# Performance work log

Measured on AMD Instinct MI355X. Metric: run time of the kernel, lower is better.

## Reference

```python
import jax, jax.numpy as jnp
import numpy as np

jax.config.update("jax_enable_x64", True)

N = 3
NX = (N ** 2) ** 3          # 729 decision vars (flattened 9x9x9 one-hot board)
M2 = 128                    # dense inequality rows (G2)
QPEN = 0.1                  # Qpenalty -> Q = QPEN * I
NITER = 10                  # fixed interior-point iterations
SIGMA = 0.1                 # centering parameter
B = 16                      # batch of puzzles


def setup_inputs() -> dict:
    key = jax.random.key(0)
    k1, k2 = jax.random.split(key)
    puzzles = jax.random.uniform(k1, (B, 9, 9, 9), dtype=jnp.float32)
    G2 = jax.random.uniform(k2, (M2, NX), minval=-1.0, maxval=1.0, dtype=jnp.float32)
    z2 = jnp.zeros((NX,), jnp.float32)
    s2 = jnp.ones((M2,), jnp.float32)
    return {"puzzles": puzzles, "G2": G2, "z2": z2, "s2": s2}


def _qp_solve(p, G2, h):
    """Solve min 0.5 z'Qz + p'z  s.t. [-I; G2] z <= h for a batch of p.

    Primal-dual interior-point method, fixed NITER steps, exploiting the
    block structure G = [-I; G2]:  G' D G = diag(d1) + G2' D2 G2.
    p: (B, NX) float64. Returns z: (B, NX).
    """
    Bn, nx = p.shape
    G = jnp.concatenate([-jnp.eye(nx, dtype=p.dtype), G2], axis=0)  # (m, nx)
    m = G.shape[0]
    eye = jnp.eye(nx, dtype=p.dtype)

    z0 = jnp.zeros((Bn, nx), p.dtype)
    s0 = jnp.ones((Bn, m), p.dtype)
    lam0 = jnp.ones((Bn, m), p.dtype)

    def maxstep(x, dx):
        # largest alpha<=1 keeping x + alpha*dx > 0 (fraction-to-boundary 0.99)
        ratio = jnp.where(dx < 0, -x / jnp.where(dx < 0, dx, -1.0), jnp.inf)
        return jnp.minimum(1.0, 0.99 * jnp.min(ratio, axis=1))

    def step(carry, _):
        z, s, lam = carry
        Gz = z @ G.T                                   # (B, m)
        rd = QPEN * z + p + lam @ G                    # dual residual (B, nx)
        rp = Gz + s - h                                # primal residual (B, m)
        mu = jnp.mean(s * lam, axis=1, keepdims=True)  # (B, 1)
        d = lam / s                                    # (B, m)
        v = SIGMA * mu / s - lam + d * rp              # (B, m)
        rhs = -(rd + v @ G)                            # (B, nx)
        # K = Q + G' D G = diag(QPEN + d1) + G2' D2 G2  (block-sparse structure)
        K = jnp.einsum('mi,bm,mj->bij', G2, d[:, nx:], G2)
        K = K + eye[None] * (QPEN + d[:, :nx])[:, :, None]
        dz = jnp.linalg.solve(K, rhs[..., None])[..., 0]
        Gdz = dz @ G.T
        ds = -rp - Gdz
        dlam = v + d * Gdz
        alpha = jnp.minimum(maxstep(s, ds), maxstep(lam, dlam))[:, None]
        return (z + alpha * dz, s + alpha * ds, lam + alpha * dlam), None

    (z, _, _), _ = jax.lax.scan(step, (z0, s0, lam0), None, length=NITER)
    return z


def reference(puzzles, G2, z2, s2):
    Bn = puzzles.shape[0]
    G2d = G2.astype(jnp.float64)
    z2d = z2.astype(jnp.float64)
    s2d = s2.astype(jnp.float64)
    p = -puzzles.reshape(Bn, -1).astype(jnp.float64)     # (B, NX)
    h2 = G2d @ z2d + s2d                                 # (M2,)
    h = jnp.concatenate([jnp.zeros(NX, jnp.float64), h2])
    z = _qp_solve(p, G2d, h)
    return z.astype(jnp.float32).reshape(puzzles.shape)
```

## Files before the change

kernel.cpp:

```cpp
#include <hip/hip_runtime.h>
#include <math.h>

#define NXQ 729
#define M2Q 128
#define MQ  857
#define BQ  16
#define QPEN_ 0.1
#define SIGMA_ 0.1

typedef double d4 __attribute__((ext_vector_type(4)));

constexpr int OFF_P    = 0;
constexpr int OFF_H2   = OFF_P + BQ*NXQ;
constexpr int OFF_Q2   = OFF_H2 + M2Q;
constexpr int OFF_TP   = OFF_Q2 + BQ*M2Q;
constexpr int ST_Z    = 0;
constexpr int ST_S    = 729;
constexpr int ST_LAM  = 1586;
constexpr int ST_RP   = 2443;
constexpr int ST_V    = 3300;
constexpr int ST_AINV = 4157;
constexpr int ST_Y    = 4886;
constexpr int ST_GZ   = 5615;
constexpr int STB     = 5743;
constexpr int OFF_ST  = OFF_TP + 12*BQ*M2Q;
constexpr int SGB_B   = 10240;
constexpr int OFF_SG  = OFF_ST + 2*BQ*STB;

constexpr int L_SL   = 0;
constexpr int L_US   = 16512;
constexpr int L_INVD = 16640;
constexpr int L_RED2 = 16768;
constexpr int SH_FUSED = (16768 + 544) * 8;
constexpr int D_DZ   = 0;
constexpr int D_RED  = 736;
constexpr int D_SC   = 744;
constexpr int D_Q2   = 752;
constexpr int D_YL   = 880;
constexpr int D_SN   = 944;
constexpr int D_LN   = 1801;
constexpr int D_PART = 2658;
constexpr int D_AINV = 12672;
constexpr int AR_W   = 1056;
constexpr int SH_PS  = 8448 * 8;

__device__ __constant__ int TRI_R[10] = {0,1,1,2,2,2,3,3,3,3};
__device__ __constant__ int TRI_C[10] = {0,0,1,0,1,2,0,1,2,3};
__device__ __constant__ int TRL_R[28] = {0,1,1,2,2,2,3,3,3,3,4,4,4,4,4,5,5,5,5,5,5,6,6,6,6,6,6,6};
__device__ __constant__ int TRL_C[28] = {0,0,1,0,1,2,0,1,2,3,0,1,2,3,4,0,1,2,3,4,5,0,1,2,3,4,5,6};

__device__ __forceinline__ double wred_sum(double v) {
#pragma unroll
  for (int off = 32; off > 0; off >>= 1) v += __shfl_down(v, off, 64);
  return v;
}
__device__ __forceinline__ double wred_min(double v) {
#pragma unroll
  for (int off = 32; off > 0; off >>= 1) v = fmin(v, __shfl_down(v, off, 64));
  return v;
}
__device__ __forceinline__ double rsqrt64(double x) {
  double r = (double)rsqrtf((float)x);
  r = r * (1.5 - 0.5 * x * r * r);
  r = r * (1.5 - 0.5 * x * r * r);
  return r;
}

__device__ __forceinline__ void mfma_cdmap(int* rowm, int* colm) {
  const int lane = threadIdx.x & 63;
  const int rc = lane & 15, kq = lane >> 4;
  const double avr = (kq == 0) ? (double)rc : 0.0;
  const double bv1 = (kq == 0) ? 1.0 : 0.0;
  const double av1 = (kq == 0) ? 1.0 : 0.0;
  const double bvc = (kq == 0) ? (double)rc : 0.0;
  d4 zero = {0.0, 0.0, 0.0, 0.0};
  d4 dr = __builtin_amdgcn_mfma_f64_16x16x4f64(avr, bv1, zero, 0, 0, 0);
  d4 dc = __builtin_amdgcn_mfma_f64_16x16x4f64(av1, bvc, zero, 0, 0, 0);
#pragma unroll
  for (int e = 0; e < 4; ++e) { rowm[e] = (int)dr[e]; colm[e] = (int)dc[e]; }
}

__global__ __launch_bounds__(512)
void init_kernel(const float* __restrict__ puzzles, const float* __restrict__ G2,
                 const float* __restrict__ z2in, const float* __restrict__ s2in,
                 double* __restrict__ ws) {
  const int blk = blockIdx.x;
  const int tid = threadIdx.x, wave = tid >> 6, lane = tid & 63;
  __shared__ double sm[32];
  if (blk < BQ) {
    const int bb = blk;
    double* st = ws + OFF_ST + bb * STB;
    for (int i = tid; i < NXQ; i += 512) {
      ws[OFF_P + bb * NXQ + i] = -(double)puzzles[bb * NXQ + i];
      st[ST_Z + i] = 0.0;
      st[ST_AINV + i] = 1.0 / (QPEN_ + 1.0);
      st[ST_RP + i] = 1.0;
      st[ST_V + i] = SIGMA_;
    }
    for (int i = tid; i < MQ; i += 512) { st[ST_S + i] = 1.0; st[ST_LAM + i] = 1.0; }
    if (tid < M2Q) st[ST_GZ + tid] = 0.0;
  } else {
    const int r = blk - 16;
    double acc = 0.0;
    for (int kx = tid; kx < NXQ; kx += 512)
      acc += (double)G2[r * NXQ + kx] * (double)z2in[kx];
    acc = wred_sum(acc);
    if (lane == 0) sm[wave] = acc;
    __syncthreads();
    if (tid == 0) {
      double t = 0.0;
#pragma unroll
      for (int w = 0; w < 8; ++w) t += sm[w];
      const double h2r = t + (double)s2in[r];
      ws[OFF_H2 + r] = h2r;
      sm[16] = h2r;
    }
    __syncthreads();
    if (tid < BQ) {
      double* st = ws + OFF_ST + tid * STB;
      const double rp2 = 1.0 - sm[16];
      st[ST_RP + NXQ + r] = rp2;
      st[ST_V  + NXQ + r] = rp2 - 0.9;
      ws[OFF_Q2 + tid * M2Q + r] = rp2 + 0.1;
    }
  }
}

__device__ __forceinline__ void sbuild_tile8(const float* __restrict__ G2,
                                             const double* __restrict__ ainv,
                                             double* __restrict__ arena,
                                             double* __restrict__ Sgb, const int tile,
                                             const int* rowm, const int* colm) {
  const int tid = threadIdx.x, wave = tid >> 6, lane = tid & 63;
  const int R0 = TRI_R[tile] * 32, C0 = TRI_C[tile] * 32;
  double* As = arena + wave * AR_W;
  double* Bs = As + 528;
  const int kw0 = wave * 92;
  const int kwend = min(kw0 + 92, NXQ);
  const int kk16 = lane & 15, rsub = lane >> 4;
  const int rc = lane & 15, kq = lane >> 4;
  d4 c00 = {0.0, 0.0, 0.0, 0.0}, c01 = c00, c10 = c00, c11 = c00;
  float pa[8], pb[8];
  {
    const int k = kw0 + kk16;
    const int kc = (k < kwend) ? k : (kwend - 1);
#pragma unroll
    for (int it = 0; it < 8; ++it) {
      const int rr = it * 4 + rsub;
      pa[it] = G2[(R0 + rr) * NXQ + kc];
      pb[it] = G2[(C0 + rr) * NXQ + kc];
    }
  }
  for (int ch = 0; ch < 6; ++ch) {
    {
      const int k = kw0 + ch * 16 + kk16;
      const bool ok = (k < kwend);
      const double aik = ok ? ainv[k] : 0.0;
#pragma unroll
      for (int it = 0; it < 8; ++it) {
        const int rr = it * 4 + rsub;
        As[kk16 * 33 + rr] = ok ? (double)pa[it] * aik : 0.0;
        Bs[kk16 * 33 + rr] = ok ? (double)pb[it] : 0.0;
      }
    }
    if (ch < 5) {
      const int k = kw0 + (ch + 1) * 16 + kk16;
      const int kc = (k < kwend) ? k : (kwend - 1);
#pragma unroll
      for (int it = 0; it < 8; ++it) {
        const int rr = it * 4 + rsub;
        pa[it] = G2[(R0 + rr) * NXQ + kc];
        pb[it] = G2[(C0 + rr) * NXQ + kc];
      }
    }
#pragma unroll
    for (int s = 0; s < 4; ++s) {
      const int ko = (s * 4 + kq) * 33;
      const double a0 = As[ko + rc], a1 = As[ko + 16 + rc];
      const double b0 = Bs[ko + rc], b1 = Bs[ko + 16 + rc];
      c00 = __builtin_amdgcn_mfma_f64_16x16x4f64(a0, b0, c00, 0, 0, 0);
      c01 = __builtin_amdgcn_mfma_f64_16x16x4f64(a0, b1, c01, 0, 0, 0);
      c10 = __builtin_amdgcn_mfma_f64_16x16x4f64(a1, b0, c10, 0, 0, 0);
      c11 = __builtin_amdgcn_mfma_f64_16x16x4f64(a1, b1, c11, 0, 0, 0);
    }
  }
  double* Wp = arena + wave * AR_W;
#pragma unroll
  for (int e = 0; e < 4; ++e) {
    Wp[rowm[e] * 33 + colm[e]]             = c00[e];
    Wp[rowm[e] * 33 + 16 + colm[e]]        = c01[e];
    Wp[(16 + rowm[e]) * 33 + colm[e]]      = c10[e];
    Wp[(16 + rowm[e]) * 33 + 16 + colm[e]] = c11[e];
  }
  __syncthreads();
  for (int idx = tid; idx < 1024; idx += 512) {
    const int r = idx >> 5, c = idx & 31;
    const int o = r * 33 + c;
    double v = arena[o];
#pragma unroll
    for (int w = 1; w < 8; ++w) v += arena[w * AR_W + o];
    Sgb[tile * 1024 + idx] = v;
  }
}

__global__ __launch_bounds__(512)
void ps_kernel(const float* __restrict__ G2, double* __restrict__ ws) {
  const int b = blockIdx.x, y = blockIdx.y;
  const int tid = threadIdx.x, lane = tid & 63;
  extern __shared__ double sm[];
  double* st = ws + OFF_ST + b * STB;
  if (y < 12) {
    double* uvec = sm;
    double* part = sm + 128;
    double* yl   = sm + 640;
    const int c0 = y * 64;
    if (tid < M2Q) uvec[tid] = ws[OFF_Q2 + b * M2Q + tid];
    __syncthreads();
    const int kk = tid & 63, rq = tid >> 6;
    const int k = c0 + kk;
    const int kg = (k < NXQ) ? k : (NXQ - 1);
    {
      const float* gp = G2 + (rq * 16) * NXQ + kg;
      double acc = 0.0;
#pragma unroll
      for (int j = 0; j < 16; ++j) acc = fma((double)gp[j * NXQ], uvec[rq * 16 + j], acc);
      part[rq * 64 + kk] = acc;
    }
    __syncthreads();
    if (tid < 64) {
      const int k2 = c0 + tid;
      double yv = 0.0;
      if (k2 < NXQ) {
        double w = 0.0;
#pragma unroll
        for (int q = 0; q < 8; ++q) w += part[q * 64 + tid];
        const double rhsk = -(QPEN_ * st[ST_Z + k2] + ws[OFF_P + b * NXQ + k2]
                              - st[ST_LAM + k2] - st[ST_V + k2] + w);
        yv = st[ST_AINV + k2] * rhsk;
        st[ST_Y + k2] = yv;
      }
      yl[tid] = yv;
    }
    __syncthreads();
    {
      const double yv = yl[lane];
      double pp[16];
#pragma unroll
      for (int jr = 0; jr < 16; ++jr)
        pp[jr] = (double)G2[((tid >> 6) * 16 + jr) * NXQ + kg] * yv;
#pragma unroll
      for (int st2 = 0; st2 < 4; ++st2) {
        const int m = 32 >> st2, half = 8 >> st2;
        const bool hi = (lane & m) != 0;
#pragma unroll
        for (int r = 0; r < 8; ++r) {
          if (r < half) {
            const double send = hi ? pp[r] : pp[r + half];
            const double recv = __shfl_xor(send, m, 64);
            pp[r] = (hi ? pp[r + half] : pp[r]) + recv;
          }
        }
      }
      double tot = pp[0];
      tot += __shfl_xor(tot, 2, 64);
      tot += __shfl_xor(tot, 1, 64);
      if ((lane & 3) == 0)
        ws[OFF_TP + (y * BQ + b) * M2Q + (tid >> 6) * 16 + ((lane >> 2) & 15)] = tot;
    }
    __syncthreads();
  }
  if (y >= 6) {
    int rowm[4], colm[4];
    mfma_cdmap(rowm, colm);
    sbuild_tile8(G2, st + ST_AINV, sm, ws + OFF_SG + b * SGB_B, y - 6,
                 rowm, colm);
  }
}

__global__ __launch_bounds__(512, 1)
void dps_kernel(const float* __restrict__ G2, double* __restrict__ ws,
                float* __restrict__ out, const int ph, const int last) {
  const int b = blockIdx.x, chunk = blockIdx.y;
  const int tid = threadIdx.x, wave = tid >> 6, lane = tid & 63;
  extern __shared__ double sm[];
  double (*Sl)[129] = (double(*)[129])(sm + L_SL);
  double* us   = sm + L_US;
  double* invd = sm + L_INVD;
  double* red2 = sm + L_RED2;
  const double* R = ws + OFF_ST + ph * BQ * STB + b * STB;
  double*       W = ws + OFF_ST + (1 - ph) * BQ * STB + b * STB;
  double* Sgb  = ws + OFF_SG + b * SGB_B;
  const int c0 = chunk * 64;

#pragma unroll
  for (int t = 0; t < 10; ++t) {
    const int R0 = TRI_R[t] * 32, C0 = TRI_C[t] * 32;
    const bool dg = (R0 == C0);
    for (int e = tid; e < 1024; e += 512) {
      const int r = e >> 5, c = e & 31;
      double v = Sgb[t * 1024 + e];
      if (dg && r == c) {
        const int i = C0 + c;
        v += R[ST_S + NXQ + i] / R[ST_LAM + NXQ + i];
      }
      Sl[R0 + r][C0 + c] = v;
    }
  }
  if (tid < M2Q) {
    double t = 0.0;
#pragma unroll
    for (int c = 0; c < 12; ++c) t += ws[OFF_TP + (c * BQ + b) * M2Q + tid];
    us[tid] = t;
  }
  __syncthreads();

  int rowm[4], colm[4];
  mfma_cdmap(rowm, colm);
  const int rc16 = lane & 15, kq4 = lane >> 4;

  auto panel16 = [&](const int K0) {
    const int r = lane;
    double a[16];
#pragma unroll
    for (int c = 0; c < 16; ++c) a[c] = Sl[K0 + r][K0 + c];
#pragma unroll
    for (int c = 0; c < 16; ++c) {
      const double dcc = __shfl(a[c], c, 64);
      const double rs = rsqrt64(dcc);
      a[c] *= rs;
      if (lane == c) invd[K0 + c] = rs;
#pragma unroll
      for (int k2 = c + 1; k2 < 16; ++k2) {
        const double lkc = __shfl(a[c], k2, 64);
        a[k2] = fma(-a[c], lkc, a[k2]);
      }
    }
#pragma unroll
    for (int c = 0; c < 16; ++c) Sl[K0 + r][K0 + c] = a[c];
  };

  auto tile_upd = [&](const int K0, const int i0, const int j0) {
    d4 tacc;
#pragma unroll
    for (int e = 0; e < 4; ++e) tacc[e] = Sl[i0 + rowm[e]][j0 + colm[e]];
#pragma unroll
    for (int m = 0; m < 4; ++m) {
      const double av = -Sl[i0 + rc16][K0 + 4 * m + kq4];
      const double bv =  Sl[j0 + rc16][K0 + 4 * m + kq4];
      tacc = __builtin_amdgcn_mfma_f64_16x16x4f64(av, bv, tacc, 0, 0, 0);
    }
#pragma unroll
    for (int e = 0; e < 4; ++e) Sl[i0 + rowm[e]][j0 + colm[e]] = tacc[e];
  };

  if (wave == 0 && lane < 16) panel16(0);
  __syncthreads();

  for (int kb = 0; kb < 8; ++kb) {
    const int K0 = kb * 16, J0 = K0 + 16, T = 128 - J0;
    if (tid <= T) {
      const bool isU = (tid == T);
      double l[16];
      if (isU) {
#pragma unroll
        for (int c = 0; c < 16; ++c) l[c] = us[K0 + c];
      } else {
#pragma unroll
        for (int c = 0; c < 16; ++c) l[c] = Sl[J0 + tid][K0 + c];
      }
#pragma unroll
      for (int c = 0; c < 16; ++c) {
        const double lc = l[c] * invd[K0 + c];
        l[c] = lc;
#pragma unroll
        for (int k2 = c + 1; k2 < 16; ++k2)
          l[k2] = fma(-lc, Sl[K0 + k2][K0 + c], l[k2]);
      }
      if (isU) {
#pragma unroll
        for (int c = 0; c < 16; ++c) us[K0 + c] = l[c];
      } else {
#pragma unroll
        for (int c = 0; c < 16; ++c) Sl[J0 + tid][K0 + c] = l[c];
      }
    }
    __syncthreads();

    if (kb < 7) {
      if (tid < T) {
        double acc = 0.0;
#pragma unroll
        for (int c = 0; c < 16; ++c) acc = fma(Sl[J0 + tid][K0 + c], us[K0 + c], acc);
        us[J0 + tid] -= acc;
      }
      if (wave == 7) tile_upd(K0, J0, J0);
      __syncthreads();
      const int Tb = 7 - kb;
      const int nt = (Tb * (Tb + 1)) >> 1;
      if (wave == 0) {
        if (lane < 16) panel16(J0);
      } else {
        for (int idx = wave; idx < nt; idx += 7)
          tile_upd(K0, J0 + TRL_R[idx] * 16, J0 + TRL_C[idx] * 16);
      }
      __syncthreads();
    }
  }

  for (int kb = 7; kb >= 0; --kb) {
    const int K0 = kb * 16;
    if (kb < 7) {
      const int c = tid & 15, ch = tid >> 4;
      double part = 0.0;
      for (int k = K0 + 16 + ch; k < 128; k += 32) part = fma(Sl[k][K0 + c], us[k], part);
      red2[ch * 17 + c] = part;
    }
    __syncthreads();
    if (wave == 0 && lane < 16) {
      const int j = lane;
      double x = us[K0 + j];
      if (kb < 7) {
        double acc = 0.0;
#pragma unroll
        for (int q = 0; q < 32; ++q) acc += red2[q * 17 + j];
        x -= acc;
      }
      double colv[16];
#pragma unroll
      for (int c = 0; c < 16; ++c) colv[c] = Sl[K0 + c][K0 + j];
      const double iv = invd[K0 + j];
#pragma unroll
      for (int cc = 0; cc < 16; ++cc) {
        const int c = 15 - cc;
        const double xiv = x * iv;
        const double uc = __shfl(xiv, c, 64);
        if (j == c) x = xiv;
        else if (j < c) x = fma(-colv[c], uc, x);
      }
      us[K0 + j] = x;
    }
    __syncthreads();
  }
  if (tid < M2Q) invd[tid] = (R[ST_S + NXQ + tid] / R[ST_LAM + NXQ + tid]) * us[tid];
  __syncthreads();
  double* g2b = invd;

  double* dzl   = sm + D_DZ;
  double* red   = sm + D_RED;
  double* sc    = sm + D_SC;
  double* ainvn = sm + D_AINV;
  double* q2l   = sm + D_Q2;
  double* yl    = sm + D_YL;
  double* snew  = sm + D_SN;
  double* lnew  = sm + D_LN;
  double* part  = sm + D_PART;

  double lmin = 1e300;
  for (int k = tid; k < NXQ; k += 512) {
    double accv = 0.0;
    const float* gp = G2 + k;
#pragma unroll 16
    for (int r = 0; r < M2Q; ++r) accv = fma((double)gp[r * NXQ], us[r], accv);
    const double dzv = R[ST_Y + k] - R[ST_AINV + k] * accv;
    dzl[k] = dzv;
    const double si = R[ST_S + k], li = R[ST_LAM + k], di = li / si;
    const double dsi = dzv - R[ST_RP + k];
    const double dlami = R[ST_V + k] - di * dzv;
    snew[k] = dsi; lnew[k] = dlami;
    if (dsi < 0.0)   lmin = fmin(lmin, -si / dsi);
    if (dlami < 0.0) lmin = fmin(lmin, -li / dlami);
  }
  if (tid >= 384) {
    const int m = tid - 384;
    const int i = NXQ + m;
    const double si = R[ST_S + i], li = R[ST_LAM + i], di = li / si;
    const double g = g2b[m];
    const double dsi = -R[ST_RP + i] - g;
    const double dlami = R[ST_V + i] + di * g;
    snew[i] = dsi; lnew[i] = dlami;
    if (dsi < 0.0)   lmin = fmin(lmin, -si / dsi);
    if (dlami < 0.0) lmin = fmin(lmin, -li / dlami);
  }
  lmin = wred_min(lmin);
  if (lane == 0) red[wave] = lmin;
  __syncthreads();
  if (tid == 0) {
    double m = red[0];
#pragma unroll
    for (int w = 1; w < 8; ++w) m = fmin(m, red[w]);
    sc[0] = fmin(1.0, 0.99 * m);
  }
  __syncthreads();
  const double alpha = sc[0];

  if (last) {
    const int k2 = c0 + (tid & 63);
    if (tid < 64 && k2 < NXQ)
      out[b * NXQ + k2] = (float)(R[ST_Z + k2] + alpha * dzl[k2]);
    return;
  }

  double musum = 0.0;
  for (int i = tid; i < MQ; i += 512) {
    const double si = R[ST_S + i], li = R[ST_LAM + i];
    const double sn = si + alpha * snew[i], ln = li + alpha * lnew[i];
    snew[i] = sn; lnew[i] = ln;
    musum += sn * ln;
  }
  musum = wred_sum(musum);
  if (lane == 0) red[wave] = musum;
  __syncthreads();
  if (tid == 0) {
    double t = 0.0;
#pragma unroll
    for (int w = 0; w < 8; ++w) t += red[w];
    sc[1] = SIGMA_ * (t / (double)MQ);
  }
  __syncthreads();
  const double smu = sc[1];

  for (int i = tid; i < MQ; i += 512) {
    const double sn = snew[i], ln = lnew[i], di = ln / sn;
    if (i < NXQ) {
      const double zn = R[ST_Z + i] + alpha * dzl[i];
      const double rpn = sn - zn;
      const double vn = smu / sn - ln + di * rpn;
      const double an = 1.0 / (QPEN_ + di);
      ainvn[i] = an;
      if ((i >> 6) == chunk) {
        W[ST_Z + i] = zn; W[ST_S + i] = sn; W[ST_LAM + i] = ln;
        W[ST_RP + i] = rpn; W[ST_V + i] = vn; W[ST_AINV + i] = an;
      }
    } else {
      const int m = i - NXQ;
      const double gzn = R[ST_GZ + m] + alpha * g2b[m];
      const double rpn = gzn + sn - ws[OFF_H2 + m];
      const double vn = smu / sn - ln + di * rpn;
      q2l[m] = ln + vn;
      if (chunk == 0) {
        W[ST_S + i] = sn; W[ST_LAM + i] = ln;
        W[ST_RP + i] = rpn; W[ST_V + i] = vn; W[ST_GZ + m] = gzn;
      }
    }
  }
  __syncthreads();

  if (chunk < 12) {
    const int kk = tid & 63, rq = tid >> 6;
    const int k = c0 + kk;
    const int kg = (k < NXQ) ? k : (NXQ - 1);
    {
      const float* gp = G2 + (rq * 16) * NXQ + kg;
      double acc = 0.0;
#pragma unroll
      for (int j = 0; j < 16; ++j) acc = fma((double)gp[j * NXQ], q2l[rq * 16 + j], acc);
      part[rq * 64 + kk] = acc;
    }
    __syncthreads();
    if (tid < 64) {
      const int k2 = c0 + tid;
      double y = 0.0;
      if (k2 < NXQ) {
        double w = 0.0;
#pragma unroll
        for (int q = 0; q < 8; ++q) w += part[q * 64 + tid];
        const double sn = snew[k2], ln = lnew[k2], di = ln / sn;
        const double zn = R[ST_Z + k2] + alpha * dzl[k2];
        const double rpn = sn - zn;
        const double vn = smu / sn - ln + di * rpn;
        const double rhsk = -(QPEN_ * zn + ws[OFF_P + b * NXQ + k2] - ln - vn + w);
        y = ainvn[k2] * rhsk;
        W[ST_Y + k2] = y;
      }
      yl[tid] = y;
    }
    __syncthreads();
    {
      const double yv = yl[lane];
      double pp[16];
#pragma unroll
      for (int jr = 0; jr < 16; ++jr)
        pp[jr] = (double)G2[((tid >> 6) * 16 + jr) * NXQ + kg] * yv;
#pragma unroll
      for (int st2 = 0; st2 < 4; ++st2) {
        const int m = 32 >> st2, half = 8 >> st2;
        const bool hi = (lane & m) != 0;
#pragma unroll
        for (int r = 0; r < 8; ++r) {
          if (r < half) {
            const double send = hi ? pp[r] : pp[r + half];
            const double recv = __shfl_xor(send, m, 64);
            pp[r] = (hi ? pp[r + half] : pp[r]) + recv;
          }
        }
      }
      double tot = pp[0];
      tot += __shfl_xor(tot, 2, 64);
      tot += __shfl_xor(tot, 1, 64);
      if ((lane & 3) == 0)
        ws[OFF_TP + (chunk * BQ + b) * M2Q + (tid >> 6) * 16 + ((lane >> 2) & 15)] = tot;
    }
    __syncthreads();
  }

  if (chunk >= 6)
    sbuild_tile8(G2, ainvn, sm, Sgb, chunk - 6, rowm, colm);
}

extern "C" void kernel_launch(void* const* d_in, const int* in_sizes, int n_in,
                              void* d_out, int out_size, void* d_ws, size_t ws_size,
                              hipStream_t stream) {
  const float* puzzles = (const float*)d_in[0];
  const float* G2      = (const float*)d_in[1];
  const float* z2      = (const float*)d_in[2];
  const float* s2      = (const float*)d_in[3];
  float* out = (float*)d_out;
  double* ws = (double*)d_ws;

  (void)hipFuncSetAttribute(reinterpret_cast<const void*>(&dps_kernel),
                            hipFuncAttributeMaxDynamicSharedMemorySize, SH_FUSED);
  (void)hipFuncSetAttribute(reinterpret_cast<const void*>(&ps_kernel),
                            hipFuncAttributeMaxDynamicSharedMemorySize, SH_PS);

  init_kernel<<<dim3(16 + M2Q), dim3(512), 0, stream>>>(puzzles, G2, z2, s2, ws);
  ps_kernel<<<dim3(BQ, 16), dim3(512), SH_PS, stream>>>(G2, ws);
  for (int it = 0; it < 10; ++it) {
    const int ph = it & 1;
    dps_kernel<<<dim3(BQ, 16), dim3(512), SH_FUSED, stream>>>(G2, ws, out, ph, (it == 9) ? 1 : 0);
  }
}
```

Before: 832.7 us.

## Widen dps_kernel to 1024 threads and spread tile updates over sixteen waves

Doubles the dps_kernel block from 512 to 1024 threads. The S-matrix load, the step-length and mu reductions, and the per-element state update become single-pass (one element per thread), and the blocked Cholesky tile updates are spread across 15 worker waves instead of 7. Several phases are guarded to the first 512 threads, and sbuild_tile8 is guarded to eight waves. Shared-memory offsets are shifted so the reduction scratch can hold 16 wave partials. The aim is more parallelism per block during the serial factorisation and elementwise phases, at the cost of register pressure from the 1024-thread bound and extra idle threads in the guarded phases.

New measurement: 1.153 ms. 1.38x slower.

```diff
diff --git a/kernel.cpp b/kernel.cpp
--- a/kernel.cpp
+++ b/kernel.cpp
@@ -34,12 +34,12 @@
 constexpr int SH_FUSED = (16768 + 544) * 8;
 constexpr int D_DZ   = 0;
 constexpr int D_RED  = 736;
-constexpr int D_SC   = 744;
-constexpr int D_Q2   = 752;
-constexpr int D_YL   = 880;
-constexpr int D_SN   = 944;
-constexpr int D_LN   = 1801;
-constexpr int D_PART = 2658;
+constexpr int D_SC   = 752;
+constexpr int D_Q2   = 760;
+constexpr int D_YL   = 888;
+constexpr int D_SN   = 952;
+constexpr int D_LN   = 1812;
+constexpr int D_PART = 2672;
 constexpr int D_AINV = 12672;
 constexpr int AR_W   = 1056;
 constexpr int SH_PS  = 8448 * 8;
@@ -133,38 +133,17 @@
                                              const int* rowm, const int* colm) {
   const int tid = threadIdx.x, wave = tid >> 6, lane = tid & 63;
   const int R0 = TRI_R[tile] * 32, C0 = TRI_C[tile] * 32;
-  double* As = arena + wave * AR_W;
-  double* Bs = As + 528;
-  const int kw0 = wave * 92;
-  const int kwend = min(kw0 + 92, NXQ);
-  const int kk16 = lane & 15, rsub = lane >> 4;
-  const int rc = lane & 15, kq = lane >> 4;
-  d4 c00 = {0.0, 0.0, 0.0, 0.0}, c01 = c00, c10 = c00, c11 = c00;
-  float pa[8], pb[8];
-  {
-    const int k = kw0 + kk16;
-    const int kc = (k < kwend) ? k : (kwend - 1);
-#pragma unroll
-    for (int it = 0; it < 8; ++it) {
-      const int rr = it * 4 + rsub;
-      pa[it] = G2[(R0 + rr) * NXQ + kc];
-      pb[it] = G2[(C0 + rr) * NXQ + kc];
-    }
-  }
-  for (int ch = 0; ch < 6; ++ch) {
+  if (wave < 8) {
+    double* As = arena + wave * AR_W;
+    double* Bs = As + 528;
+    const int kw0 = wave * 92;
+    const int kwend = min(kw0 + 92, NXQ);
+    const int kk16 = lane & 15, rsub = lane >> 4;
+    const int rc = lane & 15, kq = lane >> 4;
+    d4 c00 = {0.0, 0.0, 0.0, 0.0}, c01 = c00, c10 = c00, c11 = c00;
+    float pa[8], pb[8];
     {
-      const int k = kw0 + ch * 16 + kk16;
-      const bool ok = (k < kwend);
-      const double aik = ok ? ainv[k] : 0.0;
-#pragma unroll
-      for (int it = 0; it < 8; ++it) {
-        const int rr = it * 4 + rsub;
-        As[kk16 * 33 + rr] = ok ? (double)pa[it] * aik : 0.0;
-        Bs[kk16 * 33 + rr] = ok ? (double)pb[it] : 0.0;
-      }
-    }
-    if (ch < 5) {
-      const int k = kw0 + (ch + 1) * 16 + kk16;
+      const int k = kw0 + kk16;
       const int kc = (k < kwend) ? k : (kwend - 1);
 #pragma unroll
       for (int it = 0; it < 8; ++it) {
@@ -173,27 +152,50 @@
         pb[it] = G2[(C0 + rr) * NXQ + kc];
       }
     }
-#pragma unroll
-    for (int s = 0; s < 4; ++s) {
-      const int ko = (s * 4 + kq) * 33;
-      const double a0 = As[ko + rc], a1 = As[ko + 16 + rc];
-      const double b0 = Bs[ko + rc], b1 = Bs[ko + 16 + rc];
-      c00 = __builtin_amdgcn_mfma_f64_16x16x4f64(a0, b0, c00, 0, 0, 0);
-      c01 = __builtin_amdgcn_mfma_f64_16x16x4f64(a0, b1, c01, 0, 0, 0);
-      c10 = __builtin_amdgcn_mfma_f64_16x16x4f64(a1, b0, c10, 0, 0, 0);
-      c11 = __builtin_amdgcn_mfma_f64_16x16x4f64(a1, b1, c11, 0, 0, 0);
-    }
-  }
-  double* Wp = arena + wave * AR_W;
-#pragma unroll
-  for (int e = 0; e < 4; ++e) {
-    Wp[rowm[e] * 33 + colm[e]]             = c00[e];
-    Wp[rowm[e] * 33 + 16 + colm[e]]        = c01[e];
-    Wp[(16 + rowm[e]) * 33 + colm[e]]      = c10[e];
-    Wp[(16 + rowm[e]) * 33 + 16 + colm[e]] = c11[e];
-  }
-  __syncthreads();
-  for (int idx = tid; idx < 1024; idx += 512) {
+    for (int ch = 0; ch < 6; ++ch) {
+      {
+        const int k = kw0 + ch * 16 + kk16;
+        const bool ok = (k < kwend);
+        const double aik = ok ? ainv[k] : 0.0;
+#pragma unroll
+        for (int it = 0; it < 8; ++it) {
+          const int rr = it * 4 + rsub;
+          As[kk16 * 33 + rr] = ok ? (double)pa[it] * aik : 0.0;
+          Bs[kk16 * 33 + rr] = ok ? (double)pb[it] : 0.0;
+        }
+      }
+      if (ch < 5) {
+        const int k = kw0 + (ch + 1) * 16 + kk16;
+        const int kc = (k < kwend) ? k : (kwend - 1);
+#pragma unroll
+        for (int it = 0; it < 8; ++it) {
+          const int rr = it * 4 + rsub;
+          pa[it] = G2[(R0 + rr) * NXQ + kc];
+          pb[it] = G2[(C0 + rr) * NXQ + kc];
+        }
+      }
+#pragma unroll
+      for (int s = 0; s < 4; ++s) {
+        const int ko = (s * 4 + kq) * 33;
+        const double a0 = As[ko + rc], a1 = As[ko + 16 + rc];
+        const double b0 = Bs[ko + rc], b1 = Bs[ko + 16 + rc];
+        c00 = __builtin_amdgcn_mfma_f64_16x16x4f64(a0, b0, c00, 0, 0, 0);
+        c01 = __builtin_amdgcn_mfma_f64_16x16x4f64(a0, b1, c01, 0, 0, 0);
+        c10 = __builtin_amdgcn_mfma_f64_16x16x4f64(a1, b0, c10, 0, 0, 0);
+        c11 = __builtin_amdgcn_mfma_f64_16x16x4f64(a1, b1, c11, 0, 0, 0);
+      }
+    }
+    double* Wp = arena + wave * AR_W;
+#pragma unroll
+    for (int e = 0; e < 4; ++e) {
+      Wp[rowm[e] * 33 + colm[e]]             = c00[e];
+      Wp[rowm[e] * 33 + 16 + colm[e]]        = c01[e];
+      Wp[(16 + rowm[e]) * 33 + colm[e]]      = c10[e];
+      Wp[(16 + rowm[e]) * 33 + 16 + colm[e]] = c11[e];
+    }
+  }
+  __syncthreads();
+  for (int idx = tid; idx < 1024; idx += blockDim.x) {
     const int r = idx >> 5, c = idx & 31;
     const int o = r * 33 + c;
     double v = arena[o];
@@ -277,7 +279,8 @@
   }
 }
 
-__global__ __launch_bounds__(512, 1)
+__global__ __attribute__((amdgpu_flat_work_group_size(1024, 1024)))
+__attribute__((amdgpu_waves_per_eu(4, 4)))
 void dps_kernel(const float* __restrict__ G2, double* __restrict__ ws,
                 float* __restrict__ out, const int ph, const int last) {
   const int b = blockIdx.x, chunk = blockIdx.y;
@@ -295,16 +298,13 @@
 #pragma unroll
   for (int t = 0; t < 10; ++t) {
     const int R0 = TRI_R[t] * 32, C0 = TRI_C[t] * 32;
-    const bool dg = (R0 == C0);
-    for (int e = tid; e < 1024; e += 512) {
-      const int r = e >> 5, c = e & 31;
-      double v = Sgb[t * 1024 + e];
-      if (dg && r == c) {
-        const int i = C0 + c;
-        v += R[ST_S + NXQ + i] / R[ST_LAM + NXQ + i];
-      }
-      Sl[R0 + r][C0 + c] = v;
-    }
+    const int r = tid >> 5, c = tid & 31;
+    double v = Sgb[t * 1024 + tid];
+    if (R0 == C0 && r == c) {
+      const int i = C0 + c;
+      v += R[ST_S + NXQ + i] / R[ST_LAM + NXQ + i];
+    }
+    Sl[R0 + r][C0 + c] = v;
   }
   if (tid < M2Q) {
     double t = 0.0;
@@ -400,7 +400,7 @@
       if (wave == 0) {
         if (lane < 16) panel16(J0);
       } else {
-        for (int idx = wave; idx < nt; idx += 7)
+        for (int idx = wave; idx < nt; idx += 15)
           tile_upd(K0, J0 + TRL_R[idx] * 16, J0 + TRL_C[idx] * 16);
       }
       __syncthreads();
@@ -409,7 +409,7 @@
 
   for (int kb = 7; kb >= 0; --kb) {
     const int K0 = kb * 16;
-    if (kb < 7) {
+    if (kb < 7 && tid < 512) {
       const int c = tid & 15, ch = tid >> 4;
       double part = 0.0;
       for (int k = K0 + 16 + ch; k < 128; k += 32) part = fma(Sl[k][K0 + c], us[k], part);
@@ -456,30 +456,31 @@
   double* part  = sm + D_PART;
 
   double lmin = 1e300;
-  for (int k = tid; k < NXQ; k += 512) {
-    double accv = 0.0;
-    const float* gp = G2 + k;
+  {
+    const int k = tid;
+    if (k < NXQ) {
+      double accv = 0.0;
+      const float* gp = G2 + k;
 #pragma unroll 16
-    for (int r = 0; r < M2Q; ++r) accv = fma((double)gp[r * NXQ], us[r], accv);
-    const double dzv = R[ST_Y + k] - R[ST_AINV + k] * accv;
-    dzl[k] = dzv;
-    const double si = R[ST_S + k], li = R[ST_LAM + k], di = li / si;
-    const double dsi = dzv - R[ST_RP + k];
-    const double dlami = R[ST_V + k] - di * dzv;
-    snew[k] = dsi; lnew[k] = dlami;
-    if (dsi < 0.0)   lmin = fmin(lmin, -si / dsi);
-    if (dlami < 0.0) lmin = fmin(lmin, -li / dlami);
-  }
-  if (tid >= 384) {
-    const int m = tid - 384;
-    const int i = NXQ + m;
-    const double si = R[ST_S + i], li = R[ST_LAM + i], di = li / si;
-    const double g = g2b[m];
-    const double dsi = -R[ST_RP + i] - g;
-    const double dlami = R[ST_V + i] + di * g;
-    snew[i] = dsi; lnew[i] = dlami;
-    if (dsi < 0.0)   lmin = fmin(lmin, -si / dsi);
-    if (dlami < 0.0) lmin = fmin(lmin, -li / dlami);
+      for (int r = 0; r < M2Q; ++r) accv = fma((double)gp[r * NXQ], us[r], accv);
+      const double dzv = R[ST_Y + k] - R[ST_AINV + k] * accv;
+      dzl[k] = dzv;
+      const double si = R[ST_S + k], li = R[ST_LAM + k], di = li / si;
+      const double dsi = dzv - R[ST_RP + k];
+      const double dlami = R[ST_V + k] - di * dzv;
+      snew[k] = dsi; lnew[k] = dlami;
+      if (dsi < 0.0)   lmin = fmin(lmin, -si / dsi);
+      if (dlami < 0.0) lmin = fmin(lmin, -li / dlami);
+    } else if (k < MQ) {
+      const int m = k - NXQ;
+      const double si = R[ST_S + k], li = R[ST_LAM + k], di = li / si;
+      const double g = g2b[m];
+      const double dsi = -R[ST_RP + k] - g;
+      const double dlami = R[ST_V + k] + di * g;
+      snew[k] = dsi; lnew[k] = dlami;
+      if (dsi < 0.0)   lmin = fmin(lmin, -si / dsi);
+      if (dlami < 0.0) lmin = fmin(lmin, -li / dlami);
+    }
   }
   lmin = wred_min(lmin);
   if (lane == 0) red[wave] = lmin;
@@ -487,7 +488,7 @@
   if (tid == 0) {
     double m = red[0];
 #pragma unroll
-    for (int w = 1; w < 8; ++w) m = fmin(m, red[w]);
+    for (int w = 1; w < 16; ++w) m = fmin(m, red[w]);
     sc[0] = fmin(1.0, 0.99 * m);
   }
   __syncthreads();
@@ -500,15 +501,17 @@
     return;
   }
 
-  double musum = 0.0;
-  for (int i = tid; i < MQ; i += 512) {
-    const double si = R[ST_S + i], li = R[ST_LAM + i];
-    const double sn = si + alpha * snew[i], ln = li + alpha * lnew[i];
-    snew[i] = sn; lnew[i] = ln;
-    musum += sn * ln;
-  }
-  musum = wred_sum(musum);
-  if (lane == 0) red[wave] = musum;
+  if (tid < MQ) {
+    snew[tid] = R[ST_S + tid] + alpha * snew[tid];
+    lnew[tid] = R[ST_LAM + tid] + alpha * lnew[tid];
+  }
+  __syncthreads();
+  if (tid < 512) {
+    double musum = 0.0;
+    for (int i = tid; i < MQ; i += 512) musum += snew[i] * lnew[i];
+    musum = wred_sum(musum);
+    if (lane == 0) red[wave] = musum;
+  }
   __syncthreads();
   if (tid == 0) {
     double t = 0.0;
@@ -519,27 +522,30 @@
   __syncthreads();
   const double smu = sc[1];
 
-  for (int i = tid; i < MQ; i += 512) {
-    const double sn = snew[i], ln = lnew[i], di = ln / sn;
-    if (i < NXQ) {
-      const double zn = R[ST_Z + i] + alpha * dzl[i];
-      const double rpn = sn - zn;
-      const double vn = smu / sn - ln + di * rpn;
-      const double an = 1.0 / (QPEN_ + di);
-      ainvn[i] = an;
-      if ((i >> 6) == chunk) {
-        W[ST_Z + i] = zn; W[ST_S + i] = sn; W[ST_LAM + i] = ln;
-        W[ST_RP + i] = rpn; W[ST_V + i] = vn; W[ST_AINV + i] = an;
-      }
-    } else {
-      const int m = i - NXQ;
-      const double gzn = R[ST_GZ + m] + alpha * g2b[m];
-      const double rpn = gzn + sn - ws[OFF_H2 + m];
-      const double vn = smu / sn - ln + di * rpn;
-      q2l[m] = ln + vn;
-      if (chunk == 0) {
-        W[ST_S + i] = sn; W[ST_LAM + i] = ln;
-        W[ST_RP + i] = rpn; W[ST_V + i] = vn; W[ST_GZ + m] = gzn;
+  {
+    const int i = tid;
+    if (i < MQ) {
+      const double sn = snew[i], ln = lnew[i], di = ln / sn;
+      if (i < NXQ) {
+        const double zn = R[ST_Z + i] + alpha * dzl[i];
+        const double rpn = sn - zn;
+        const double vn = smu / sn - ln + di * rpn;
+        const double an = 1.0 / (QPEN_ + di);
+        ainvn[i] = an;
+        if ((i >> 6) == chunk) {
+          W[ST_Z + i] = zn; W[ST_S + i] = sn; W[ST_LAM + i] = ln;
+          W[ST_RP + i] = rpn; W[ST_V + i] = vn; W[ST_AINV + i] = an;
+        }
+      } else {
+        const int m = i - NXQ;
+        const double gzn = R[ST_GZ + m] + alpha * g2b[m];
+        const double rpn = gzn + sn - ws[OFF_H2 + m];
+        const double vn = smu / sn - ln + di * rpn;
+        q2l[m] = ln + vn;
+        if (chunk == 0) {
+          W[ST_S + i] = sn; W[ST_LAM + i] = ln;
+          W[ST_RP + i] = rpn; W[ST_V + i] = vn; W[ST_GZ + m] = gzn;
+        }
       }
     }
   }
@@ -549,7 +555,7 @@
     const int kk = tid & 63, rq = tid >> 6;
     const int k = c0 + kk;
     const int kg = (k < NXQ) ? k : (NXQ - 1);
-    {
+    if (tid < 512) {
       const float* gp = G2 + (rq * 16) * NXQ + kg;
       double acc = 0.0;
 #pragma unroll
@@ -575,7 +581,7 @@
       yl[tid] = y;
     }
     __syncthreads();
-    {
+    if (tid < 512) {
       const double yv = yl[lane];
       double pp[16];
 #pragma unroll
@@ -626,6 +632,6 @@
   ps_kernel<<<dim3(BQ, 16), dim3(512), SH_PS, stream>>>(G2, ws);
   for (int it = 0; it < 10; ++it) {
     const int ph = it & 1;
-    dps_kernel<<<dim3(BQ, 16), dim3(512), SH_FUSED, stream>>>(G2, ws, out, ph, (it == 9) ? 1 : 0);
-  }
-}
+    dps_kernel<<<dim3(BQ, 16), dim3(1024), SH_FUSED, stream>>>(G2, ws, out, ph, (it == 9) ? 1 : 0);
+  }
+}
```

## Pack Schur matrix lower-triangular and split S-build into halves across more blocks

Applied to the files above, without the earlier changes.

The 128x128 Schur complement is now stored in packed lower-triangular form in LDS, roughly halving shared memory per block so launch bounds can allow four blocks per CU. The S-build work is split into two K-halves, each using four waves, and is spread over twice as many blocks (grid y 16 to 32), with the halves summed when the matrix is assembled. The S-build and ps/dps chunks become disjoint branches instead of overlapping in the same block. In exchange, packed-index arithmetic adds address cost, half the waves sit idle during S-build, and more global partial sums are written and read.

Measured after the change: 1.482 ms. 1.78x slower.

```diff
diff --git a/kernel.cpp b/kernel.cpp
--- a/kernel.cpp
+++ b/kernel.cpp
@@ -24,30 +24,37 @@
 constexpr int ST_GZ   = 5615;
 constexpr int STB     = 5743;
 constexpr int OFF_ST  = OFF_TP + 12*BQ*M2Q;
-constexpr int SGB_B   = 10240;
+constexpr int SGB_B   = 20480;
 constexpr int OFF_SG  = OFF_ST + 2*BQ*STB;
 
 constexpr int L_SL   = 0;
-constexpr int L_US   = 16512;
-constexpr int L_INVD = 16640;
-constexpr int L_RED2 = 16768;
-constexpr int SH_FUSED = (16768 + 544) * 8;
+constexpr int L_US   = 8256;
+constexpr int L_INVD = 8384;
+constexpr int L_RED2 = 8512;
+constexpr int SH_FUSED = (8512 + 544) * 8;
 constexpr int D_DZ   = 0;
-constexpr int D_RED  = 736;
-constexpr int D_SC   = 744;
-constexpr int D_Q2   = 752;
-constexpr int D_YL   = 880;
-constexpr int D_SN   = 944;
-constexpr int D_LN   = 1801;
-constexpr int D_PART = 2658;
-constexpr int D_AINV = 12672;
+constexpr int D_SN   = 736;
+constexpr int D_LN   = 1596;
+constexpr int D_PART = 2456;
+constexpr int D_Q2   = 2968;
+constexpr int D_YL   = 3096;
+constexpr int D_RED  = 3160;
+constexpr int D_SC   = 3168;
 constexpr int AR_W   = 1056;
-constexpr int SH_PS  = 8448 * 8;
+constexpr int D_AINV = 4224;
+constexpr int SH_PS  = (704 + 4224) * 8;
 
 __device__ __constant__ int TRI_R[10] = {0,1,1,2,2,2,3,3,3,3};
 __device__ __constant__ int TRI_C[10] = {0,0,1,0,1,2,0,1,2,3};
 __device__ __constant__ int TRL_R[28] = {0,1,1,2,2,2,3,3,3,3,4,4,4,4,4,5,5,5,5,5,5,6,6,6,6,6,6,6};
 __device__ __constant__ int TRL_C[28] = {0,0,1,0,1,2,0,1,2,3,0,1,2,3,4,0,1,2,3,4,5,0,1,2,3,4,5,6};
+
+__device__ __forceinline__ int PX(const int r, const int c) {
+  return ((r * (r + 1)) >> 1) + c;
+}
+__device__ __forceinline__ int PXS(const int r, const int c) {
+  return (r >= c) ? PX(r, c) : PX(c, r);
+}
 
 __device__ __forceinline__ double wred_sum(double v) {
 #pragma unroll
@@ -126,45 +133,25 @@
   }
 }
 
-__device__ __forceinline__ void sbuild_tile8(const float* __restrict__ G2,
-                                             const double* __restrict__ ainv,
-                                             double* __restrict__ arena,
-                                             double* __restrict__ Sgb, const int tile,
-                                             const int* rowm, const int* colm) {
+__device__ __forceinline__ void sbuild_half(const float* __restrict__ G2,
+                                            const double* __restrict__ ainv,
+                                            double* __restrict__ arena,
+                                            double* __restrict__ Sgb,
+                                            const int tile, const int half,
+                                            const int* rowm, const int* colm) {
   const int tid = threadIdx.x, wave = tid >> 6, lane = tid & 63;
   const int R0 = TRI_R[tile] * 32, C0 = TRI_C[tile] * 32;
-  double* As = arena + wave * AR_W;
-  double* Bs = As + 528;
-  const int kw0 = wave * 92;
-  const int kwend = min(kw0 + 92, NXQ);
-  const int kk16 = lane & 15, rsub = lane >> 4;
-  const int rc = lane & 15, kq = lane >> 4;
-  d4 c00 = {0.0, 0.0, 0.0, 0.0}, c01 = c00, c10 = c00, c11 = c00;
-  float pa[8], pb[8];
-  {
-    const int k = kw0 + kk16;
-    const int kc = (k < kwend) ? k : (kwend - 1);
-#pragma unroll
-    for (int it = 0; it < 8; ++it) {
-      const int rr = it * 4 + rsub;
-      pa[it] = G2[(R0 + rr) * NXQ + kc];
-      pb[it] = G2[(C0 + rr) * NXQ + kc];
-    }
-  }
-  for (int ch = 0; ch < 6; ++ch) {
+  if (wave < 4) {
+    double* As = arena + wave * AR_W;
+    double* Bs = As + 528;
+    const int kw0 = half * 368 + wave * 92;
+    const int kwend = min(kw0 + 92, NXQ);
+    const int kk16 = lane & 15, rsub = lane >> 4;
+    const int rc = lane & 15, kq = lane >> 4;
+    d4 c00 = {0.0, 0.0, 0.0, 0.0}, c01 = c00, c10 = c00, c11 = c00;
+    float pa[8], pb[8];
     {
-      const int k = kw0 + ch * 16 + kk16;
-      const bool ok = (k < kwend);
-      const double aik = ok ? ainv[k] : 0.0;
-#pragma unroll
-      for (int it = 0; it < 8; ++it) {
-        const int rr = it * 4 + rsub;
-        As[kk16 * 33 + rr] = ok ? (double)pa[it] * aik : 0.0;
-        Bs[kk16 * 33 + rr] = ok ? (double)pb[it] : 0.0;
-      }
-    }
-    if (ch < 5) {
-      const int k = kw0 + (ch + 1) * 16 + kk16;
+      const int k = kw0 + kk16;
       const int kc = (k < kwend) ? k : (kwend - 1);
 #pragma unroll
       for (int it = 0; it < 8; ++it) {
@@ -173,37 +160,58 @@
         pb[it] = G2[(C0 + rr) * NXQ + kc];
       }
     }
-#pragma unroll
-    for (int s = 0; s < 4; ++s) {
-      const int ko = (s * 4 + kq) * 33;
-      const double a0 = As[ko + rc], a1 = As[ko + 16 + rc];
-      const double b0 = Bs[ko + rc], b1 = Bs[ko + 16 + rc];
-      c00 = __builtin_amdgcn_mfma_f64_16x16x4f64(a0, b0, c00, 0, 0, 0);
-      c01 = __builtin_amdgcn_mfma_f64_16x16x4f64(a0, b1, c01, 0, 0, 0);
-      c10 = __builtin_amdgcn_mfma_f64_16x16x4f64(a1, b0, c10, 0, 0, 0);
-      c11 = __builtin_amdgcn_mfma_f64_16x16x4f64(a1, b1, c11, 0, 0, 0);
-    }
-  }
-  double* Wp = arena + wave * AR_W;
-#pragma unroll
-  for (int e = 0; e < 4; ++e) {
-    Wp[rowm[e] * 33 + colm[e]]             = c00[e];
-    Wp[rowm[e] * 33 + 16 + colm[e]]        = c01[e];
-    Wp[(16 + rowm[e]) * 33 + colm[e]]      = c10[e];
-    Wp[(16 + rowm[e]) * 33 + 16 + colm[e]] = c11[e];
+    for (int ch = 0; ch < 6; ++ch) {
+      {
+        const int k = kw0 + ch * 16 + kk16;
+        const bool ok = (k < kwend);
+        const double aik = ok ? ainv[k] : 0.0;
+#pragma unroll
+        for (int it = 0; it < 8; ++it) {
+          const int rr = it * 4 + rsub;
+          As[kk16 * 33 + rr] = ok ? (double)pa[it] * aik : 0.0;
+          Bs[kk16 * 33 + rr] = ok ? (double)pb[it] : 0.0;
+        }
+      }
+      if (ch < 5) {
+        const int k = kw0 + (ch + 1) * 16 + kk16;
+        const int kc = (k < kwend) ? k : (kwend - 1);
+#pragma unroll
+        for (int it = 0; it < 8; ++it) {
+          const int rr = it * 4 + rsub;
+          pa[it] = G2[(R0 + rr) * NXQ + kc];
+          pb[it] = G2[(C0 + rr) * NXQ + kc];
+        }
+      }
+#pragma unroll
+      for (int s = 0; s < 4; ++s) {
+        const int ko = (s * 4 + kq) * 33;
+        const double a0 = As[ko + rc], a1 = As[ko + 16 + rc];
+        const double b0 = Bs[ko + rc], b1 = Bs[ko + 16 + rc];
+        c00 = __builtin_amdgcn_mfma_f64_16x16x4f64(a0, b0, c00, 0, 0, 0);
+        c01 = __builtin_amdgcn_mfma_f64_16x16x4f64(a0, b1, c01, 0, 0, 0);
+        c10 = __builtin_amdgcn_mfma_f64_16x16x4f64(a1, b0, c10, 0, 0, 0);
+        c11 = __builtin_amdgcn_mfma_f64_16x16x4f64(a1, b1, c11, 0, 0, 0);
+      }
+    }
+    double* Wp = arena + wave * AR_W;
+#pragma unroll
+    for (int e = 0; e < 4; ++e) {
+      Wp[rowm[e] * 33 + colm[e]]             = c00[e];
+      Wp[rowm[e] * 33 + 16 + colm[e]]        = c01[e];
+      Wp[(16 + rowm[e]) * 33 + colm[e]]      = c10[e];
+      Wp[(16 + rowm[e]) * 33 + 16 + colm[e]] = c11[e];
+    }
   }
   __syncthreads();
   for (int idx = tid; idx < 1024; idx += 512) {
     const int r = idx >> 5, c = idx & 31;
     const int o = r * 33 + c;
-    double v = arena[o];
-#pragma unroll
-    for (int w = 1; w < 8; ++w) v += arena[w * AR_W + o];
-    Sgb[tile * 1024 + idx] = v;
-  }
-}
-
-__global__ __launch_bounds__(512)
+    const double v = arena[o] + arena[AR_W + o] + arena[2*AR_W + o] + arena[3*AR_W + o];
+    Sgb[(tile * 2 + half) * 1024 + idx] = v;
+  }
+}
+
+__global__ __launch_bounds__(512, 4)
 void ps_kernel(const float* __restrict__ G2, double* __restrict__ ws) {
   const int b = blockIdx.x, y = blockIdx.y;
   const int tid = threadIdx.x, lane = tid & 63;
@@ -267,23 +275,22 @@
       if ((lane & 3) == 0)
         ws[OFF_TP + (y * BQ + b) * M2Q + (tid >> 6) * 16 + ((lane >> 2) & 15)] = tot;
     }
-    __syncthreads();
-  }
-  if (y >= 6) {
+  } else {
     int rowm[4], colm[4];
     mfma_cdmap(rowm, colm);
-    sbuild_tile8(G2, st + ST_AINV, sm, ws + OFF_SG + b * SGB_B, y - 6,
-                 rowm, colm);
-  }
-}
-
-__global__ __launch_bounds__(512, 1)
+    const int u = y - 12;
+    sbuild_half(G2, st + ST_AINV, sm + 704, ws + OFF_SG + b * SGB_B,
+                u >> 1, u & 1, rowm, colm);
+  }
+}
+
+__global__ __launch_bounds__(512, 4)
 void dps_kernel(const float* __restrict__ G2, double* __restrict__ ws,
                 float* __restrict__ out, const int ph, const int last) {
   const int b = blockIdx.x, chunk = blockIdx.y;
   const int tid = threadIdx.x, wave = tid >> 6, lane = tid & 63;
   extern __shared__ double sm[];
-  double (*Sl)[129] = (double(*)[129])(sm + L_SL);
+  double* P    = sm + L_SL;
   double* us   = sm + L_US;
   double* invd = sm + L_INVD;
   double* red2 = sm + L_RED2;
@@ -298,12 +305,13 @@
     const bool dg = (R0 == C0);
     for (int e = tid; e < 1024; e += 512) {
       const int r = e >> 5, c = e & 31;
-      double v = Sgb[t * 1024 + e];
+      if (dg && c > r) continue;
+      double v = Sgb[(t * 2) * 1024 + e] + Sgb[(t * 2 + 1) * 1024 + e];
       if (dg && r == c) {
         const int i = C0 + c;
         v += R[ST_S + NXQ + i] / R[ST_LAM + NXQ + i];
       }
-      Sl[R0 + r][C0 + c] = v;
+      P[PX(R0 + r, C0 + c)] = v;
     }
   }
   if (tid < M2Q) {
@@ -322,7 +330,7 @@
     const int r = lane;
     double a[16];
 #pragma unroll
-    for (int c = 0; c < 16; ++c) a[c] = Sl[K0 + r][K0 + c];
+    for (int c = 0; c < 16; ++c) a[c] = P[PXS(K0 + r, K0 + c)];
 #pragma unroll
     for (int c = 0; c < 16; ++c) {
       const double dcc = __shfl(a[c], c, 64);
@@ -336,21 +344,26 @@
       }
     }
 #pragma unroll
-    for (int c = 0; c < 16; ++c) Sl[K0 + r][K0 + c] = a[c];
+    for (int c = 0; c < 16; ++c)
+      if (c <= r) P[PX(K0 + r, K0 + c)] = a[c];
   };
 
   auto tile_upd = [&](const int K0, const int i0, const int j0) {
     d4 tacc;
 #pragma unroll
-    for (int e = 0; e < 4; ++e) tacc[e] = Sl[i0 + rowm[e]][j0 + colm[e]];
+    for (int e = 0; e < 4; ++e)
+      tacc[e] = P[PXS(i0 + rowm[e], j0 + colm[e])];
 #pragma unroll
     for (int m = 0; m < 4; ++m) {
-      const double av = -Sl[i0 + rc16][K0 + 4 * m + kq4];
-      const double bv =  Sl[j0 + rc16][K0 + 4 * m + kq4];
+      const double av = -P[PX(i0 + rc16, K0 + 4 * m + kq4)];
+      const double bv =  P[PX(j0 + rc16, K0 + 4 * m + kq4)];
       tacc = __builtin_amdgcn_mfma_f64_16x16x4f64(av, bv, tacc, 0, 0, 0);
     }
 #pragma unroll
-    for (int e = 0; e < 4; ++e) Sl[i0 + rowm[e]][j0 + colm[e]] = tacc[e];
+    for (int e = 0; e < 4; ++e) {
+      const int rr = i0 + rowm[e], cc = j0 + colm[e];
+      if (rr >= cc) P[PX(rr, cc)] = tacc[e];
+    }
   };
 
   if (wave == 0 && lane < 16) panel16(0);
@@ -366,7 +379,7 @@
         for (int c = 0; c < 16; ++c) l[c] = us[K0 + c];
       } else {
 #pragma unroll
-        for (int c = 0; c < 16; ++c) l[c] = Sl[J0 + tid][K0 + c];
+        for (int c = 0; c < 16; ++c) l[c] = P[PX(J0 + tid, K0 + c)];
       }
 #pragma unroll
       for (int c = 0; c < 16; ++c) {
@@ -374,14 +387,14 @@
         l[c] = lc;
 #pragma unroll
         for (int k2 = c + 1; k2 < 16; ++k2)
-          l[k2] = fma(-lc, Sl[K0 + k2][K0 + c], l[k2]);
+          l[k2] = fma(-lc, P[PX(K0 + k2, K0 + c)], l[k2]);
       }
       if (isU) {
 #pragma unroll
         for (int c = 0; c < 16; ++c) us[K0 + c] = l[c];
       } else {
 #pragma unroll
-        for (int c = 0; c < 16; ++c) Sl[J0 + tid][K0 + c] = l[c];
+        for (int c = 0; c < 16; ++c) P[PX(J0 + tid, K0 + c)] = l[c];
       }
     }
     __syncthreads();
@@ -390,7 +403,7 @@
       if (tid < T) {
         double acc = 0.0;
 #pragma unroll
-        for (int c = 0; c < 16; ++c) acc = fma(Sl[J0 + tid][K0 + c], us[K0 + c], acc);
+        for (int c = 0; c < 16; ++c) acc = fma(P[PX(J0 + tid, K0 + c)], us[K0 + c], acc);
         us[J0 + tid] -= acc;
       }
       if (wave == 7) tile_upd(K0, J0, J0);
@@ -412,7 +425,7 @@
     if (kb < 7) {
       const int c = tid & 15, ch = tid >> 4;
       double part = 0.0;
-      for (int k = K0 + 16 + ch; k < 128; k += 32) part = fma(Sl[k][K0 + c], us[k], part);
+      for (int k = K0 + 16 + ch; k < 128; k += 32) part = fma(P[PX(k, K0 + c)], us[k], part);
       red2[ch * 17 + c] = part;
     }
     __syncthreads();
@@ -427,7 +440,7 @@
       }
       double colv[16];
 #pragma unroll
-      for (int c = 0; c < 16; ++c) colv[c] = Sl[K0 + c][K0 + j];
+      for (int c = 0; c < 16; ++c) colv[c] = P[PXS(K0 + c, K0 + j)];
       const double iv = invd[K0 + j];
 #pragma unroll
       for (int cc = 0; cc < 16; ++cc) {
@@ -600,11 +613,10 @@
       if ((lane & 3) == 0)
         ws[OFF_TP + (chunk * BQ + b) * M2Q + (tid >> 6) * 16 + ((lane >> 2) & 15)] = tot;
     }
-    __syncthreads();
-  }
-
-  if (chunk >= 6)
-    sbuild_tile8(G2, ainvn, sm, Sgb, chunk - 6, rowm, colm);
+  } else {
+    const int u = chunk - 12;
+    sbuild_half(G2, ainvn, sm, Sgb, u >> 1, u & 1, rowm, colm);
+  }
 }
 
 extern "C" void kernel_launch(void* const* d_in, const int* in_sizes, int n_in,
@@ -623,9 +635,9 @@
                             hipFuncAttributeMaxDynamicSharedMemorySize, SH_PS);
 
   init_kernel<<<dim3(16 + M2Q), dim3(512), 0, stream>>>(puzzles, G2, z2, s2, ws);
-  ps_kernel<<<dim3(BQ, 16), dim3(512), SH_PS, stream>>>(G2, ws);
+  ps_kernel<<<dim3(BQ, 32), dim3(512), SH_PS, stream>>>(G2, ws);
   for (int it = 0; it < 10; ++it) {
     const int ph = it & 1;
-    dps_kernel<<<dim3(BQ, 16), dim3(512), SH_FUSED, stream>>>(G2, ws, out, ph, (it == 9) ? 1 : 0);
-  }
-}
+    dps_kernel<<<dim3(BQ, 32), dim3(512), SH_FUSED, stream>>>(G2, ws, out, ph, (it == 9) ? 1 : 0);
+  }
+}
```
